# Optimization experiments

Hardware: AMD Instinct MI355X
Metric: run time of the kernel (lower is better)

The kernel has to match this reference:

```python
import jax, jax.numpy as jnp
import numpy as np

NUM_RAYS = 131072
NUM_EXISTING = 256
NUM_SAMPLES = 96
NEAR, FAR = 2.0, 6.0


def setup_inputs() -> dict:
    key = jax.random.key(0)
    k_w, = jax.random.split(key, 1)
    weights = jax.random.uniform(k_w, (NUM_RAYS, NUM_EXISTING, 1), dtype=jnp.float32)
    # existing bins: uniform partition of [0,1] in normalized spacing coordinates
    edges = jnp.linspace(0.0, 1.0, NUM_EXISTING + 1, dtype=jnp.float32)
    spacing_starts = jnp.broadcast_to(edges[:-1, None], (NUM_RAYS, NUM_EXISTING, 1))
    spacing_ends = jnp.broadcast_to(edges[1:, None], (NUM_RAYS, NUM_EXISTING, 1))
    return {
        "weights": weights,
        "spacing_starts": spacing_starts,
        "spacing_ends": spacing_ends,
        "num_samples": NUM_SAMPLES,
    }


def _pdf_sample(weights, spacing_starts, spacing_ends, num_samples, eps=1e-5):
    num_bins = num_samples + 1  # static Python int
    w = weights[..., 0]                                   # [R, N]
    w_sum = jnp.sum(w, axis=-1, keepdims=True)            # [R, 1]
    padding = jax.nn.relu(eps - w_sum)
    w = w + padding / w.shape[-1]
    w_sum = w_sum + padding
    pdf = w / w_sum
    cdf = jnp.minimum(jnp.ones_like(pdf), jnp.cumsum(pdf, axis=-1))
    cdf = jnp.concatenate([jnp.zeros_like(cdf[..., :1]), cdf], axis=-1)  # [R, N+1]

    # eval path: deterministic bin midpoints in CDF space
    u = jnp.linspace(0.0, 1.0 - 1.0 / num_bins, num_bins, dtype=cdf.dtype)
    u = u + 1.0 / (2 * num_bins)
    u = jnp.broadcast_to(u, (*cdf.shape[:-1], num_bins))   # [R, num_bins]

    existing_bins = jnp.concatenate(
        [spacing_starts[..., 0], spacing_ends[..., -1:, 0]], axis=-1
    )                                                       # [R, N+1]

    # per-ray binary search (right bisection), vmapped over rays
    inds = jax.vmap(lambda c, uu: jnp.searchsorted(c, uu, side="right"))(cdf, u)
    last = existing_bins.shape[-1] - 1
    below = jnp.clip(inds - 1, 0, last)
    above = jnp.clip(inds, 0, last)

    cdf_g0 = jnp.take_along_axis(cdf, below, axis=-1)
    bins_g0 = jnp.take_along_axis(existing_bins, below, axis=-1)
    cdf_g1 = jnp.take_along_axis(cdf, above, axis=-1)
    bins_g1 = jnp.take_along_axis(existing_bins, above, axis=-1)

    denom = cdf_g1 - cdf_g0
    denom = jnp.where(denom < 1e-5, jnp.ones_like(denom), denom)
    t = jnp.clip((u - cdf_g0) / denom, 0.0, 1.0)
    bins = bins_g0 + t * (bins_g1 - bins_g0)
    bins = jax.lax.stop_gradient(bins)  # .detach() in original

    euclidean_bins = NEAR + bins * (FAR - NEAR)  # spacing_to_euclidean_fn (linear)
    # stack [euclidean_bins, spacing_bins]: [2, R, num_bins]
    return jnp.stack([euclidean_bins, bins], axis=0)


def reference(weights, spacing_starts, spacing_ends, num_samples):
    return _pdf_sample(weights, spacing_starts, spacing_ends, num_samples)
```

## Files before the change

kernel.cpp:

```cpp
#include <hip/hip_runtime.h>


#define NUM_RAYS 131072
#define NUM_EXISTING 256
#define NUM_BINS 97
#define NEAR_T 2.0f
#define FAR_T 6.0f
#define EPS_W 1e-5f

constexpr int WAVES_PER_BLOCK = 4;
constexpr int BLOCK = 64 * WAVES_PER_BLOCK;
constexpr int ROW = NUM_EXISTING + 4;

__global__ __launch_bounds__(BLOCK) void pdf_sample_kernel(
    const float* __restrict__ weights,
    const float* __restrict__ spacing_starts,
    const float* __restrict__ spacing_ends,
    float* __restrict__ out)
{
    __shared__ float s_cdf[WAVES_PER_BLOCK][ROW];
    __shared__ float s_bin[WAVES_PER_BLOCK][ROW];

    const int wave = threadIdx.x >> 6;
    const int lane = threadIdx.x & 63;
    const int ray  = blockIdx.x * WAVES_PER_BLOCK + wave;

    const float* wrow = weights        + (size_t)ray * NUM_EXISTING;
    const float* srow = spacing_starts + (size_t)ray * NUM_EXISTING;

    float4 w4 = reinterpret_cast<const float4*>(wrow)[lane];
    float4 b4 = reinterpret_cast<const float4*>(srow)[lane];

    float* cdfw = s_cdf[wave];
    float* binw = s_bin[wave];

    reinterpret_cast<float4*>(binw)[lane] = b4;
    if (lane == 0) {
        binw[NUM_EXISTING] = spacing_ends[(size_t)ray * NUM_EXISTING + (NUM_EXISTING - 1)];
        cdfw[0] = 0.0f;
    }

    float sl   = (w4.x + w4.y) + (w4.z + w4.w);
    float incl = sl;
    #pragma unroll
    for (int off = 1; off < 64; off <<= 1) {
        float n = __shfl_up(incl, off);
        if (lane >= off) incl += n;
    }
    float total = __shfl(incl, 63);
    float excl  = incl - sl;

    float padding  = fmaxf(EPS_W - total, 0.0f);
    float pad_each = padding * (1.0f / (float)NUM_EXISTING);
    float inv      = 1.0f / (total + padding);

    float base = (excl + (float)(lane * 4) * pad_each) * inv;
    float p0 = (w4.x + pad_each) * inv;
    float p1 = (w4.y + pad_each) * inv;
    float p2 = (w4.z + pad_each) * inv;
    float p3 = (w4.w + pad_each) * inv;
    float c0 = base + p0;
    float c1 = c0 + p1;
    float c2 = c1 + p2;
    float c3 = c2 + p3;

    int ci = 1 + lane * 4;
    cdfw[ci + 0] = fminf(c0, 1.0f);
    cdfw[ci + 1] = fminf(c1, 1.0f);
    cdfw[ci + 2] = fminf(c2, 1.0f);
    cdfw[ci + 3] = fminf(c3, 1.0f);

    __syncthreads();

    float* out_e = out + (size_t)ray * NUM_BINS;
    float* out_s = out + (size_t)NUM_RAYS * NUM_BINS + (size_t)ray * NUM_BINS;

    constexpr float U_STEP = 1.0f / (float)NUM_BINS;
    constexpr float U_HALF = 0.5f / (float)NUM_BINS;

    #pragma unroll
    for (int it = 0; it < 2; ++it) {
        int j = lane + it * 64;
        if (j < NUM_BINS) {
            float u = fmaf((float)j, U_STEP, U_HALF);

            int lo = 0, hi = NUM_EXISTING + 1;
            while (lo < hi) {
                int mid = (lo + hi) >> 1;
                if (cdfw[mid] <= u) lo = mid + 1; else hi = mid;
            }
            int below = lo - 1; if (below < 0) below = 0; if (below > NUM_EXISTING) below = NUM_EXISTING;
            int above = lo;     if (above > NUM_EXISTING) above = NUM_EXISTING;

            float cg0 = cdfw[below];
            float cg1 = cdfw[above];
            float bg0 = binw[below];
            float bg1 = binw[above];

            float denom = cg1 - cg0;
            denom = (denom < 1e-5f) ? 1.0f : denom;
            float t = (u - cg0) / denom;
            t = fminf(fmaxf(t, 0.0f), 1.0f);

            float bins = fmaf(t, bg1 - bg0, bg0);
            float eucl = fmaf(bins, (FAR_T - NEAR_T), NEAR_T);

            out_e[j] = eucl;
            out_s[j] = bins;
        }
    }
}

extern "C" void kernel_launch(void* const* d_in, const int* in_sizes, int n_in,
                              void* d_out, int out_size, void* d_ws, size_t ws_size,
                              hipStream_t stream) {
    const float* weights        = (const float*)d_in[0];
    const float* spacing_starts = (const float*)d_in[1];
    const float* spacing_ends   = (const float*)d_in[2];
    float* out = (float*)d_out;

    dim3 grid(NUM_RAYS / WAVES_PER_BLOCK);
    dim3 block(BLOCK);
    pdf_sample_kernel<<<grid, block, 0, stream>>>(weights, spacing_starts, spacing_ends, out);
}
```

Before: 353.5 us.

## Replace per-sample binary search with LDS histogram and prefix-scan searchsorted

```diff
diff --git a/kernel.cpp b/kernel.cpp
--- a/kernel.cpp
+++ b/kernel.cpp
@@ -4,13 +4,13 @@
 #define NUM_RAYS 131072
 #define NUM_EXISTING 256
 #define NUM_BINS 97
-#define NEAR_T 2.0f
-#define FAR_T 6.0f
 #define EPS_W 1e-5f
 
 constexpr int WAVES_PER_BLOCK = 4;
 constexpr int BLOCK = 64 * WAVES_PER_BLOCK;
-constexpr int ROW = NUM_EXISTING + 4;
+constexpr int ROW  = NUM_EXISTING + 4;
+constexpr int CROW = NUM_EXISTING + 4;
+constexpr int HROW = 128;
 
 __global__ __launch_bounds__(BLOCK) void pdf_sample_kernel(
     const float* __restrict__ weights,
@@ -18,8 +18,9 @@
     const float* __restrict__ spacing_ends,
     float* __restrict__ out)
 {
-    __shared__ float s_cdf[WAVES_PER_BLOCK][ROW];
-    __shared__ float s_bin[WAVES_PER_BLOCK][ROW];
+    __shared__ __align__(16) float s_bin[WAVES_PER_BLOCK][ROW];
+    __shared__ __align__(16) float s_cdf[WAVES_PER_BLOCK][CROW];
+    __shared__ __align__(16) int   s_h[WAVES_PER_BLOCK][HROW];
 
     const int wave = threadIdx.x >> 6;
     const int lane = threadIdx.x & 63;
@@ -31,14 +32,16 @@
     float4 w4 = reinterpret_cast<const float4*>(wrow)[lane];
     float4 b4 = reinterpret_cast<const float4*>(srow)[lane];
 
+    float* binw = s_bin[wave];
     float* cdfw = s_cdf[wave];
-    float* binw = s_bin[wave];
+    int*   hw   = s_h[wave];
 
     reinterpret_cast<float4*>(binw)[lane] = b4;
-    if (lane == 0) {
+    if (lane == 0)
         binw[NUM_EXISTING] = spacing_ends[(size_t)ray * NUM_EXISTING + (NUM_EXISTING - 1)];
-        cdfw[0] = 0.0f;
-    }
+
+    hw[lane]      = 0;
+    hw[lane + 64] = 0;
 
     float sl   = (w4.x + w4.y) + (w4.z + w4.w);
     float incl = sl;
@@ -55,22 +58,34 @@
     float inv      = 1.0f / (total + padding);
 
     float base = (excl + (float)(lane * 4) * pad_each) * inv;
-    float p0 = (w4.x + pad_each) * inv;
-    float p1 = (w4.y + pad_each) * inv;
-    float p2 = (w4.z + pad_each) * inv;
-    float p3 = (w4.w + pad_each) * inv;
-    float c0 = base + p0;
-    float c1 = c0 + p1;
-    float c2 = c1 + p2;
-    float c3 = c2 + p3;
+    float cc = base + (w4.x + pad_each) * inv;  float c0 = fminf(cc, 1.0f);
+    cc += (w4.y + pad_each) * inv;              float c1 = fminf(cc, 1.0f);
+    cc += (w4.z + pad_each) * inv;              float c2 = fminf(cc, 1.0f);
+    cc += (w4.w + pad_each) * inv;              float c3 = fminf(cc, 1.0f);
 
-    int ci = 1 + lane * 4;
-    cdfw[ci + 0] = fminf(c0, 1.0f);
-    cdfw[ci + 1] = fminf(c1, 1.0f);
-    cdfw[ci + 2] = fminf(c2, 1.0f);
-    cdfw[ci + 3] = fminf(c3, 1.0f);
+    float4 cst = make_float4(c0, c1, c2, c3);
+    reinterpret_cast<float4*>(cdfw)[lane] = cst;
 
-    __syncthreads();
+    #pragma unroll
+    for (int k = 0; k < 4; ++k) {
+        float c = (k == 0) ? c0 : (k == 1) ? c1 : (k == 2) ? c2 : c3;
+        int m = (int)ceilf(fmaf(97.0f, c, -0.5f));
+        m = m < 0 ? 0 : (m > 97 ? 97 : m);
+        atomicAdd(&hw[m], 1);
+    }
+
+    int2 hp = *reinterpret_cast<const int2*>(&hw[2 * lane]);
+    int v0 = hp.x, v1 = hp.y;
+    int ps = v0 + v1;
+    int pincl = ps;
+    #pragma unroll
+    for (int off = 1; off < 64; off <<= 1) {
+        int n = __shfl_up(pincl, off);
+        if (lane >= off) pincl += n;
+    }
+    int pexcl = pincl - ps;
+    int inds0 = 1 + pexcl + v0;
+    int inds1 = inds0 + v1;
 
     float* out_e = out + (size_t)ray * NUM_BINS;
     float* out_s = out + (size_t)NUM_RAYS * NUM_BINS + (size_t)ray * NUM_BINS;
@@ -79,33 +94,32 @@
     constexpr float U_HALF = 0.5f / (float)NUM_BINS;
 
     #pragma unroll
-    for (int it = 0; it < 2; ++it) {
-        int j = lane + it * 64;
+    for (int k = 0; k < 2; ++k) {
+        int j = 2 * lane + k;
         if (j < NUM_BINS) {
+            int idx   = (k == 0) ? inds0 : inds1;
+            idx       = idx > 256 ? 256 : idx;
+            int below = idx - 1;
+
             float u = fmaf((float)j, U_STEP, U_HALF);
 
-            int lo = 0, hi = NUM_EXISTING + 1;
-            while (lo < hi) {
-                int mid = (lo + hi) >> 1;
-                if (cdfw[mid] <= u) lo = mid + 1; else hi = mid;
-            }
-            int below = lo - 1; if (below < 0) below = 0; if (below > NUM_EXISTING) below = NUM_EXISTING;
-            int above = lo;     if (above > NUM_EXISTING) above = NUM_EXISTING;
+            int cb = below - 1; cb = cb < 0 ? 0 : cb;
+            float x = cdfw[cb];
+            float y = cdfw[cb + 1];
+            float cg0 = (below == 0) ? 0.0f : x;
+            float cg1 = (below == 0) ? x    : y;
 
-            float cg0 = cdfw[below];
-            float cg1 = cdfw[above];
             float bg0 = binw[below];
-            float bg1 = binw[above];
+            float bg1 = binw[below + 1];
 
             float denom = cg1 - cg0;
             denom = (denom < 1e-5f) ? 1.0f : denom;
-            float t = (u - cg0) / denom;
+            float t = __fdividef(u - cg0, denom);
             t = fminf(fmaxf(t, 0.0f), 1.0f);
 
             float bins = fmaf(t, bg1 - bg0, bg0);
-            float eucl = fmaf(bins, (FAR_T - NEAR_T), NEAR_T);
 
-            out_e[j] = eucl;
+            out_e[j] = fmaf(bins, 4.0f, 2.0f);
             out_s[j] = bins;
         }
     }
```

After: 353.3 us. About the same (-0.1%).
